# Kernel tuning notes

Measured on AMD Instinct MI355X. Metric: run time of the kernel, lower is better.

The kernel has to match this reference:

```python
import jax, jax.numpy as jnp
import numpy as np
from jax import lax

DG = 8  # deformable groups


def conv3(x, w, b):
    # 3x3 stride-1 SAME conv, NCHW/OIHW
    y = lax.conv_general_dilated(x, w, (1, 1), 'SAME',
                                 dimension_numbers=('NCHW', 'OIHW', 'NCHW'))
    return y + b[None, :, None, None]


def lrelu(x):
    return jnp.where(x >= 0, x, 0.1 * x)


def _mdcn(x, offset, mask, w, b, dg):
    """Modulated deformable conv v2: 3x3, stride 1, pad 1, dilation 1, groups 1.
    offset: [B, 2*dg*9, H, W] (first dg*9 = y offsets, second dg*9 = x offsets),
    mask:   [B, dg*9, H, W] (already sigmoided)."""
    B, C, H, W = x.shape
    kk = 9
    Cg = C // dg
    off = offset.reshape(B, 2, dg, kk, H, W)
    oy, ox = off[:, 0], off[:, 1]            # [B, dg, kk, H, W]
    m = mask.reshape(B, dg, kk, H, W)
    ky = (jnp.arange(kk) // 3 - 1).astype(x.dtype).reshape(1, 1, kk, 1, 1)
    kx = (jnp.arange(kk) % 3 - 1).astype(x.dtype).reshape(1, 1, kk, 1, 1)
    hg = jnp.arange(H, dtype=x.dtype).reshape(1, 1, 1, H, 1)
    wg = jnp.arange(W, dtype=x.dtype).reshape(1, 1, 1, 1, W)
    py = hg + ky + oy                        # sampling positions (pad=1 cancels k-1 shift)
    px = wg + kx + ox
    y0 = jnp.floor(py)
    x0 = jnp.floor(px)
    wy = py - y0
    wx = px - x0
    xg = x.reshape(B, dg, Cg, H * W)
    acc = jnp.zeros((B, dg, Cg, kk, H, W), x.dtype)
    for dy, dx, wgt in ((0.0, 0.0, (1 - wy) * (1 - wx)),
                        (0.0, 1.0, (1 - wy) * wx),
                        (1.0, 0.0, wy * (1 - wx)),
                        (1.0, 1.0, wy * wx)):
        yy = y0 + dy
        xx = x0 + dx
        valid = (yy >= 0) & (yy < H) & (xx >= 0) & (xx < W)
        yi = jnp.clip(yy, 0, H - 1).astype(jnp.int32)
        xi = jnp.clip(xx, 0, W - 1).astype(jnp.int32)
        idx = (yi * W + xi).reshape(B, dg, 1, kk * H * W)
        v = jnp.take_along_axis(xg, idx, axis=3).reshape(B, dg, Cg, kk, H, W)
        acc = acc + v * (wgt * valid.astype(x.dtype))[:, :, None]
    acc = acc * m[:, :, None]                # modulation mask
    sampled = acc.reshape(B, C, kk, H, W)
    out = jnp.einsum('bckhw,ock->bohw', sampled, w.reshape(w.shape[0], C, kk))
    return out + b[None, :, None, None]


def _dcn_pack(x, feat, w_om, b_om, w, b):
    out = conv3(feat, w_om, b_om)            # [B, 3*dg*9, H, W]
    o1, o2, mr = jnp.split(out, 3, axis=1)
    offset = jnp.concatenate([o1, o2], axis=1)
    mask = jax.nn.sigmoid(mr)
    return _mdcn(x, offset, mask, w, b, DG)


def _forward(ref, neb,
             w_oc1, b_oc1, w_om1, b_om1, w_dcn1, b_dcn1, w_fc, b_fc,
             w_cas1, b_cas1, w_cas2, b_cas2, w_om2, b_om2, w_dcn2, b_dcn2,
             w_ta1, b_ta1, w_ta2, b_ta2, w_ff, b_ff):
    start = ref
    # --- PCD alignment (nbr_feat_l = neb, ref_feat_l = ref) ---
    off = lrelu(conv3(jnp.concatenate([neb, ref], axis=1), w_oc1, b_oc1))
    feat = _dcn_pack(neb, off, w_om1, b_om1, w_dcn1, b_dcn1)
    feat = lrelu(conv3(feat, w_fc, b_fc))
    off = jnp.concatenate([feat, ref], axis=1)
    off = lrelu(conv3(lrelu(conv3(off, w_cas1, b_cas1)), w_cas2, b_cas2))
    feat = lrelu(_dcn_pack(feat, off, w_om2, b_om2, w_dcn2, b_dcn2))
    # --- TSA fusion (ref=ref, neb=feat) ---
    emb_ref = conv3(ref, w_ta1, b_ta1)
    emb = conv3(feat, w_ta2, b_ta2)
    corr = jnp.sum(emb * emb_ref, axis=1, keepdims=True)  # [B,1,H,W]
    feat = lrelu(conv3(ref * corr, w_ff, b_ff))
    return feat + start


def setup_inputs() -> dict:
    key = jax.random.key(0)
    ks = jax.random.split(key, 32)
    B, C, H, W = 4, 64, 180, 320
    s = 0.05
    p = lambda k, shape: (jax.random.normal(k, shape, jnp.float32) * s)
    OM = 3 * DG * 9  # 216
    return {
        'ref': jax.random.normal(ks[0], (B, C, H, W), jnp.float32),
        'neb': jax.random.normal(ks[1], (B, C, H, W), jnp.float32),
        'w_oc1': p(ks[2], (C, 2 * C, 3, 3)), 'b_oc1': p(ks[3], (C,)),
        'w_om1': p(ks[4], (OM, C, 3, 3)),    'b_om1': p(ks[5], (OM,)),
        'w_dcn1': p(ks[6], (C, C, 3, 3)),    'b_dcn1': p(ks[7], (C,)),
        'w_fc': p(ks[8], (C, C, 3, 3)),      'b_fc': p(ks[9], (C,)),
        'w_cas1': p(ks[10], (C, 2 * C, 3, 3)), 'b_cas1': p(ks[11], (C,)),
        'w_cas2': p(ks[12], (C, C, 3, 3)),   'b_cas2': p(ks[13], (C,)),
        'w_om2': p(ks[14], (OM, C, 3, 3)),   'b_om2': p(ks[15], (OM,)),
        'w_dcn2': p(ks[16], (C, C, 3, 3)),   'b_dcn2': p(ks[17], (C,)),
        'w_ta1': p(ks[18], (C, C, 3, 3)),    'b_ta1': p(ks[19], (C,)),
        'w_ta2': p(ks[20], (C, C, 3, 3)),    'b_ta2': p(ks[21], (C,)),
        'w_ff': p(ks[22], (C, C, 3, 3)),     'b_ff': p(ks[23], (C,)),
    }


def reference(ref, neb,
              w_oc1, b_oc1, w_om1, b_om1, w_dcn1, b_dcn1, w_fc, b_fc,
              w_cas1, b_cas1, w_cas2, b_cas2, w_om2, b_om2, w_dcn2, b_dcn2,
              w_ta1, b_ta1, w_ta2, b_ta2, w_ff, b_ff):
    return _forward(ref, neb,
                    w_oc1, b_oc1, w_om1, b_om1, w_dcn1, b_dcn1, w_fc, b_fc,
                    w_cas1, b_cas1, w_cas2, b_cas2, w_om2, b_om2, w_dcn2, b_dcn2,
                    w_ta1, b_ta1, w_ta2, b_ta2, w_ff, b_ff)
```

## Files before the change

### kernel.cpp

```cpp
#include <hip/hip_runtime.h>
#include <cmath>


using short8 = __attribute__((ext_vector_type(8))) short;
using f32x4  = __attribute__((ext_vector_type(4))) float;

#define DEVINL static __device__ __forceinline__

DEVINL unsigned short f2bf(float f){
    unsigned u = __float_as_uint(f);
    u += 0x7fffu + ((u >> 16) & 1u);
    return (unsigned short)(u >> 16);
}
DEVINL unsigned pack2(float a, float b){ return (unsigned)f2bf(a) | ((unsigned)f2bf(b) << 16); }
DEVINL float bflo(unsigned u){ return __uint_as_float(u << 16); }
DEVINL float bfhi(unsigned u){ return __uint_as_float(u & 0xffff0000u); }
DEVINL float bf2f(unsigned short u){ return __uint_as_float((unsigned)u << 16); }
DEVINL float lrelu_f(float v){ return v >= 0.f ? v : 0.1f * v; }

DEVINL void swz_decode(int& bx, int& by, int& bz){
    const int gx = gridDim.x, gy = gridDim.y;
    int lin = blockIdx.x + gx * (blockIdx.y + gy * blockIdx.z);
    int nwg = gx * gy * gridDim.z;
    int q = nwg >> 3, r = nwg & 7;
    int xcd = lin & 7, idx = lin >> 3;
    int swz = (xcd < r ? xcd * (q + 1) : r + xcd * q) + idx;
    bz = swz / (gx * gy);
    int rem = swz - bz * gx * gy;
    by = rem / gx; bx = rem - by * gx;
}

struct Ptr4 { unsigned short* p[4]; };

__global__ __launch_bounds__(256) void nchw2nhwc2(const float* __restrict__ inA,
                                                  const float* __restrict__ inB,
                                                  unsigned short* __restrict__ outA,
                                                  unsigned short* __restrict__ outB)
{
    constexpr int HW = 180 * 320;
    const int blk = blockIdx.x;
    const float* in = (blk < 900) ? inA : inB;
    unsigned short* out = (blk < 900) ? outA : outB;
    size_t idx = (size_t)(blk % 900) * 256 + threadIdx.x;
    size_t bb = idx / HW, p = idx % HW;
    const float* src = in + (bb * 64) * (size_t)HW + p;
    unsigned short* dst = out + idx * 64;
    #pragma unroll
    for (int c0 = 0; c0 < 64; c0 += 16) {
        unsigned r[8];
        #pragma unroll
        for (int q = 0; q < 8; ++q)
            r[q] = pack2(src[(size_t)(c0 + 2*q) * HW], src[(size_t)(c0 + 2*q + 1) * HW]);
        *(uint4*)(dst + c0)     = *(uint4*)&r[0];
        *(uint4*)(dst + c0 + 8) = *(uint4*)&r[4];
    }
}

struct PrepArgs {
    const float* src[11];
    unsigned short* dst[11];
    int cout[11]; int cin[11]; int nch[11]; int kind[11];
};

__global__ __launch_bounds__(256) void prep_all(PrepArgs a)
{
    const int t = blockIdx.y;
    const int idx = blockIdx.x * 256 + threadIdx.x;
    if (a.kind[t] == 1) {
        if (idx >= 36864) return;
        int kk = idx & 31, oc = (idx >> 5) & 63, s = idx >> 11;
        int k = s * 32 + kk;
        int gt = k >> 3, c8 = k & 7;
        int g = gt / 9, tp = gt - g * 9;
        a.dst[t][idx] = f2bf(a.src[t][((size_t)oc * 64 + g * 8 + c8) * 9 + tp]);
    } else {
        int cin = a.cin[t], cout = a.cout[t];
        int ncs = cin / 32;
        int total = a.nch[t] * 9 * ncs * 2048;
        if (idx >= total) return;
        int kk = idx & 31, oc_l = (idx >> 5) & 63, rest = idx >> 11;
        int cs = rest % ncs; int rest2 = rest / ncs;
        int j = rest2 % 9; int ch = rest2 / 9;
        int oc = ch * 64 + oc_l, c = cs * 32 + kk;
        float v = (oc < cout) ? a.src[t][((size_t)oc * cin + c) * 9 + j] : 0.f;
        a.dst[t][idx] = f2bf(v);
    }
}

template<int CIN, bool TWO_IN, bool ACT, bool SCALE, int OUTMODE, int NM>
__global__ __launch_bounds__(256, (CIN == 128 ? 2 : 3)) void conv_mfma(
    const unsigned short* __restrict__ in0, const unsigned short* __restrict__ in1,
    const unsigned short* __restrict__ wgt, const float* __restrict__ bias,
    unsigned short* __restrict__ out, const float* __restrict__ corr,
    const float* __restrict__ res, float* __restrict__ outf,
    Ptr4 omout, int choff, int zdiv, int COUT)
{
    constexpr int H = 180, W = 320, HW = H * W;
    constexpr int NCB = CIN / 8;
    constexpr int NCS = CIN / 32;
    __shared__ __align__(16) unsigned char lds[6 * 34 * CIN * 2];

    const int tid = threadIdx.x;
    int bx, by, bz;
    swz_decode(bx, by, bz);
    int b, ch;
    if (OUTMODE == 1) { b = bz / zdiv; ch = bz % zdiv + choff; }
    else              { b = bz; ch = 0; }
    const int x0 = bx * 32, y0 = by * 4;

    for (int t = tid; t < 6 * 34 * NCB; t += 256) {
        int cb = t % NCB; int r = t / NCB;
        int xp = r % 34, yp = r / 34;
        int gx = x0 - 1 + xp, gy = y0 - 1 + yp;
        uint4 v = make_uint4(0, 0, 0, 0);
        if (gx >= 0 && gx < W && gy >= 0 && gy < H) {
            size_t pix = (size_t)b * HW + (size_t)gy * W + gx;
            const unsigned short* src;
            if (TWO_IN) src = (cb < 8) ? (in0 + pix * 64 + cb * 8) : (in1 + pix * 64 + (cb - 8) * 8);
            else        src = in0 + pix * CIN + cb * 8;
            v = *(const uint4*)src;
            if (SCALE) {
                float cv = corr[pix];
                v.x = pack2(bflo(v.x) * cv, bfhi(v.x) * cv);
                v.y = pack2(bflo(v.y) * cv, bfhi(v.y) * cv);
                v.z = pack2(bflo(v.z) * cv, bfhi(v.z) * cv);
                v.w = pack2(bflo(v.w) * cv, bfhi(v.w) * cv);
            }
        }
        int blk = cb ^ (xp & 7);
        *(uint4*)&lds[(size_t)((yp * 34 + xp) * NCB + blk) * 16] = v;
    }
    __syncthreads();

    const int wv = tid >> 6, lane = tid & 63;
    const int ll = lane & 15, lh = lane >> 4;
    const unsigned short* wchunk = wgt + (size_t)ch * (9 * NCS * 2048);
    const int alane = ll * 32 + lh * 8;

    f32x4 acc[NM][2];
    #pragma unroll
    for (int mi = 0; mi < NM; ++mi)
        #pragma unroll
        for (int nf = 0; nf < 2; ++nf) acc[mi][nf] = f32x4{0.f, 0.f, 0.f, 0.f};

    #pragma unroll
    for (int j = 0; j < 9; ++j) {
        const int jy = j / 3, jx = j % 3;
        #pragma unroll
        for (int cs = 0; cs < NCS; ++cs) {
            const int s = j * NCS + cs;
            short8 a[NM];
            #pragma unroll
            for (int mi = 0; mi < NM; ++mi)
                a[mi] = *(const short8*)(wchunk + (size_t)s * 2048 + mi * 512 + alane);
            short8 bf[2];
            #pragma unroll
            for (int nf = 0; nf < 2; ++nf) {
                int xp = nf * 16 + ll + jx;
                int blk = (cs * 4 + lh) ^ (xp & 7);
                int addr = (((wv + jy) * 34 + xp) * NCB + blk) * 16;
                bf[nf] = *(const short8*)&lds[addr];
            }
            #pragma unroll
            for (int mi = 0; mi < NM; ++mi)
                #pragma unroll
                for (int nf = 0; nf < 2; ++nf)
                    acc[mi][nf] = __builtin_amdgcn_mfma_f32_16x16x32_bf16(a[mi], bf[nf], acc[mi][nf], 0, 0, 0);
        }
    }

    const int py = y0 + wv;
    const size_t pixrow = (size_t)b * HW + (size_t)py * W;
    #pragma unroll
    for (int nf = 0; nf < 2; ++nf) {
        const int px = x0 + nf * 16 + ll;
        if (OUTMODE == 3) {
            float dot = 0.f;
            const unsigned* er = (const unsigned*)(in1 + (pixrow + px) * 64);
            #pragma unroll
            for (int mi = 0; mi < NM; ++mi) {
                const int oc_l = mi * 16 + lh * 4;
                unsigned e0 = er[oc_l / 2], e1 = er[oc_l / 2 + 1];
                float t0 = acc[mi][nf][0] + bias[oc_l + 0];
                float t1 = acc[mi][nf][1] + bias[oc_l + 1];
                float t2 = acc[mi][nf][2] + bias[oc_l + 2];
                float t3 = acc[mi][nf][3] + bias[oc_l + 3];
                dot += t0 * bflo(e0) + t1 * bfhi(e0) + t2 * bflo(e1) + t3 * bfhi(e1);
            }
            dot += __shfl_xor(dot, 16);
            dot += __shfl_xor(dot, 32);
            if (lh == 0) outf[pixrow + px] = dot;
        } else if (OUTMODE == 1) {
            unsigned short* oslot = omout.p[b];
            #pragma unroll
            for (int mi = 0; mi < NM; ++mi) {
                const int oc_l = mi * 16 + lh * 4;
                #pragma unroll
                for (int jj = 0; jj < 4; ++jj) {
                    int ocg = ch * 64 + oc_l + jj;
                    if (ocg < COUT) {
                        float t = acc[mi][nf][jj] + bias[ocg];
                        oslot[(size_t)ocg * HW + (size_t)py * W + px] = f2bf(ACT ? lrelu_f(t) : t);
                    }
                }
            }
        } else {
            #pragma unroll
            for (int mi = 0; mi < NM; ++mi) {
                const int oc_l = mi * 16 + lh * 4;
                if (OUTMODE == 0) {
                    float v[4];
                    #pragma unroll
                    for (int jj = 0; jj < 4; ++jj) {
                        float t = acc[mi][nf][jj] + bias[oc_l + jj];
                        v[jj] = ACT ? lrelu_f(t) : t;
                    }
                    uint2 st; st.x = pack2(v[0], v[1]); st.y = pack2(v[2], v[3]);
                    *(uint2*)&out[(pixrow + px) * 64 + oc_l] = st;
                } else {
                    #pragma unroll
                    for (int jj = 0; jj < 4; ++jj) {
                        int oc = oc_l + jj;
                        float t = acc[mi][nf][jj] + bias[oc];
                        if (ACT) t = lrelu_f(t);
                        size_t idx = ((size_t)b * 64 + oc) * HW + (size_t)py * W + px;
                        outf[idx] = t + res[idx];
                    }
                }
            }
        }
    }
}

template<int ACT>
__global__ __launch_bounds__(256, 4) void mdcn_mfma(
    const unsigned short* __restrict__ x, size_t xstride,
    const unsigned short* __restrict__ om, size_t omstride,
    const unsigned short* __restrict__ wgt, const float* __restrict__ bias,
    unsigned short* __restrict__ out, size_t ostride)
{
    constexpr int H = 180, W = 320, HW = H * W;
    __shared__ __align__(16) unsigned char sv[72 * 32 * 16];

    const int tid = threadIdx.x;
    int bx, by, bz;
    swz_decode(bx, by, bz);
    const unsigned short* xb  = x  + (size_t)bz * xstride;
    const unsigned short* omb = om + (size_t)bz * omstride;
    unsigned short* ob        = out + (size_t)bz * ostride;
    const int px0 = bx * 32;
    const int py  = by;

    {
        const int pxl = tid & 31, g = tid >> 5;
        const int px = px0 + pxl;
        const size_t p = (size_t)py * W + px;
        const unsigned short* omg = omb + (size_t)(g * 9) * HW + p;

        float oyv[9], oxv[9], mmv[9];
        #pragma unroll
        for (int k = 0; k < 9; ++k) oyv[k] = bf2f(omg[(size_t)k * HW]);
        #pragma unroll
        for (int k = 0; k < 9; ++k) oxv[k] = bf2f(omg[(size_t)(72 + k) * HW]);
        #pragma unroll
        for (int k = 0; k < 9; ++k) mmv[k] = bf2f(omg[(size_t)(144 + k) * HW]);

        #pragma unroll
        for (int k = 0; k < 9; ++k) {
            float m = 1.f / (1.f + __expf(-mmv[k]));
            float pyf = (float)(py + (k / 3) - 1) + oyv[k];
            float pxf = (float)(px + (k % 3) - 1) + oxv[k];
            float y0f = floorf(pyf), x0f = floorf(pxf);
            float wy = pyf - y0f, wx = pxf - x0f;
            int yi = (int)y0f, xi = (int)x0f;
            bool vy0 = (yi >= 0) && (yi < H);
            bool vy1 = (yi + 1 >= 0) && (yi + 1 < H);
            bool vx0 = (xi >= 0) && (xi < W);
            bool vx1 = (xi + 1 >= 0) && (xi + 1 < W);
            float w00 = (vy0 && vx0) ? (1.f - wy) * (1.f - wx) * m : 0.f;
            float w01 = (vy0 && vx1) ? (1.f - wy) * wx * m : 0.f;
            float w10 = (vy1 && vx0) ? wy * (1.f - wx) * m : 0.f;
            float w11 = (vy1 && vx1) ? wy * wx * m : 0.f;
            int yc0 = min(max(yi, 0), H - 1), yc1 = min(max(yi + 1, 0), H - 1);
            int xc0 = min(max(xi, 0), W - 1), xc1 = min(max(xi + 1, 0), W - 1);
            uint4 c00 = *(const uint4*)(xb + ((size_t)(yc0 * W + xc0) * 64 + g * 8));
            uint4 c01 = *(const uint4*)(xb + ((size_t)(yc0 * W + xc1) * 64 + g * 8));
            uint4 c10 = *(const uint4*)(xb + ((size_t)(yc1 * W + xc0) * 64 + g * 8));
            uint4 c11 = *(const uint4*)(xb + ((size_t)(yc1 * W + xc1) * 64 + g * 8));
            const unsigned* p00 = (const unsigned*)&c00;
            const unsigned* p01 = (const unsigned*)&c01;
            const unsigned* p10 = (const unsigned*)&c10;
            const unsigned* p11 = (const unsigned*)&c11;
            unsigned r[4];
            #pragma unroll
            for (int q = 0; q < 4; ++q) {
                float lo = w00 * bflo(p00[q]) + w01 * bflo(p01[q]) + w10 * bflo(p10[q]) + w11 * bflo(p11[q]);
                float hi = w00 * bfhi(p00[q]) + w01 * bfhi(p01[q]) + w10 * bfhi(p10[q]) + w11 * bfhi(p11[q]);
                r[q] = pack2(lo, hi);
            }
            *(uint4*)&sv[(size_t)((g * 9 + k) * 32 + pxl) * 16] = *(uint4*)r;
        }
    }
    __syncthreads();

    const int wv = tid >> 6, lane = tid & 63;
    const int ll = lane & 15, lh = lane >> 4;
    f32x4 acc[2] = {f32x4{0.f,0.f,0.f,0.f}, f32x4{0.f,0.f,0.f,0.f}};
    #pragma unroll
    for (int s = 0; s < 18; ++s) {
        short8 a = *(const short8*)(wgt + (size_t)(s * 64 + wv * 16 + ll) * 32 + lh * 8);
        #pragma unroll
        for (int nf = 0; nf < 2; ++nf) {
            short8 bb = *(const short8*)&sv[(size_t)s * 2048 + lh * 512 + (nf * 16 + ll) * 16];
            acc[nf] = __builtin_amdgcn_mfma_f32_16x16x32_bf16(a, bb, acc[nf], 0, 0, 0);
        }
    }
    #pragma unroll
    for (int nf = 0; nf < 2; ++nf) {
        int opx = px0 + nf * 16 + ll;
        int oc0 = wv * 16 + lh * 4;
        float v[4];
        #pragma unroll
        for (int jj = 0; jj < 4; ++jj) {
            float t = acc[nf][jj] + bias[oc0 + jj];
            v[jj] = ACT ? lrelu_f(t) : t;
        }
        uint2 st; st.x = pack2(v[0], v[1]); st.y = pack2(v[2], v[3]);
        *(uint2*)&ob[((size_t)py * W + opx) * 64 + oc0] = st;
    }
}

extern "C" void kernel_launch(void* const* d_in, const int* in_sizes, int n_in,
                              void* d_out, int out_size, void* d_ws, size_t ws_size,
                              hipStream_t stream)
{
    const float* ref    = (const float*)d_in[0];
    const float* neb    = (const float*)d_in[1];
    const float* w_oc1  = (const float*)d_in[2];  const float* b_oc1  = (const float*)d_in[3];
    const float* w_om1  = (const float*)d_in[4];  const float* b_om1  = (const float*)d_in[5];
    const float* w_dcn1 = (const float*)d_in[6];  const float* b_dcn1 = (const float*)d_in[7];
    const float* w_fc   = (const float*)d_in[8];  const float* b_fc   = (const float*)d_in[9];
    const float* w_cas1 = (const float*)d_in[10]; const float* b_cas1 = (const float*)d_in[11];
    const float* w_cas2 = (const float*)d_in[12]; const float* b_cas2 = (const float*)d_in[13];
    const float* w_om2  = (const float*)d_in[14]; const float* b_om2  = (const float*)d_in[15];
    const float* w_dcn2 = (const float*)d_in[16]; const float* b_dcn2 = (const float*)d_in[17];
    const float* w_ta1  = (const float*)d_in[18]; const float* b_ta1  = (const float*)d_in[19];
    const float* w_ta2  = (const float*)d_in[20]; const float* b_ta2  = (const float*)d_in[21];
    const float* w_ff   = (const float*)d_in[22]; const float* b_ff   = (const float*)d_in[23];

    constexpr int H = 180, W = 320, HW = H * W;
    constexpr size_t CHW = (size_t)HW * 64;
    constexpr size_t SLB = 4 * CHW * 2;
    constexpr size_t OMSLOT_EL = (size_t)HW * 216;
    constexpr size_t OMSLOT_B  = OMSLOT_EL * 2;

    char* wsb = (char*)d_ws;
    unsigned short* S0 = (unsigned short*)(wsb);
    unsigned short* S1 = (unsigned short*)(wsb + SLB);
    unsigned short* S2 = (unsigned short*)(wsb + 2 * SLB);
    unsigned short* S3 = (unsigned short*)(wsb + 3 * SLB);
    float* corrf = (float*)S3;
    unsigned short* ffw = (unsigned short*)(wsb + SLB + (2u << 20));

    char* doutb = (char*)d_out;
    unsigned short* omA0 = (unsigned short*)doutb;
    unsigned short* omA1 = omA0 + OMSLOT_EL;
    unsigned short* wb   = (unsigned short*)(doutb + 2 * OMSLOT_B);
    const bool big = ws_size >= 4 * SLB + 2 * OMSLOT_B;
    unsigned short* omB0 = (unsigned short*)(wsb + 4 * SLB);
    unsigned short* omB1 = omB0 + OMSLOT_EL;

    unsigned short* w_oc1p = wb + 0;
    unsigned short* w_om1p = wb + 73728;
    unsigned short* w_dcn1p= wb + 221184;
    unsigned short* w_fcp  = wb + 258048;
    unsigned short* w_cas1p= wb + 294912;
    unsigned short* w_cas2p= wb + 368640;
    unsigned short* w_om2p = wb + 405504;
    unsigned short* w_dcn2p= wb + 552960;
    unsigned short* w_ta1p = wb + 589824;
    unsigned short* w_ta2p = wb + 626688;
    unsigned short* w_ffp  = wb + 663552;

    dim3 blk(256);
    dim3 g4(10, 45, 4);
    dim3 gm(10, 180, 2);
    Ptr4 none{};

    nchw2nhwc2<<<1800, blk, 0, stream>>>(ref, neb, S0, S1);

    {
        PrepArgs pa;
        const float* srcs[11] = {w_oc1, w_om1, w_dcn1, w_fc, w_cas1, w_cas2, w_om2, w_dcn2, w_ta1, w_ta2, w_ff};
        unsigned short* dsts[11] = {w_oc1p, w_om1p, w_dcn1p, w_fcp, w_cas1p, w_cas2p, w_om2p, w_dcn2p, w_ta1p, w_ta2p, w_ffp};
        int couts[11] = {64, 216, 0, 64, 64, 64, 216, 0, 64, 64, 64};
        int cins[11]  = {128, 64, 0, 64, 128, 64, 64, 0, 64, 64, 64};
        int nchs[11]  = {1, 4, 0, 1, 1, 1, 4, 0, 1, 1, 1};
        int kinds[11] = {0, 0, 1, 0, 0, 0, 0, 1, 0, 0, 0};
        for (int i = 0; i < 11; ++i) {
            pa.src[i] = srcs[i]; pa.dst[i] = dsts[i];
            pa.cout[i] = couts[i]; pa.cin[i] = cins[i]; pa.nch[i] = nchs[i]; pa.kind[i] = kinds[i];
        }
        prep_all<<<dim3(576, 11), blk, 0, stream>>>(pa);
    }

    conv_mfma<128, true, true, false, 0, 4><<<g4, blk, 0, stream>>>(
        S1, S0, w_oc1p, b_oc1, S2, nullptr, nullptr, nullptr, none, 0, 1, 64);

    auto ompack = [&](const unsigned short* inp, const unsigned short* wp, const float* bp,
                      Ptr4 slots, int nb){
        conv_mfma<64, false, false, false, 1, 4><<<dim3(10, 45, 3 * nb), blk, 0, stream>>>(
            inp, nullptr, wp, bp, nullptr, nullptr, nullptr, nullptr, slots, 0, 3, 216);
        conv_mfma<64, false, false, false, 1, 2><<<dim3(10, 45, nb), blk, 0, stream>>>(
            inp, nullptr, wp, bp, nullptr, nullptr, nullptr, nullptr, slots, 3, 1, 216);
    };

    if (big) {
        Ptr4 slots{omA0, omA1, omB0, omB1};
        ompack(S2, w_om1p, b_om1, slots, 4);
        mdcn_mfma<0><<<gm, blk, 0, stream>>>(S1, CHW, omA0, OMSLOT_EL, w_dcn1p, b_dcn1, S3, CHW);
        mdcn_mfma<0><<<gm, blk, 0, stream>>>(S1 + 2 * CHW, CHW, omB0, OMSLOT_EL, w_dcn1p, b_dcn1, S3 + 2 * CHW, CHW);
    } else {
        Ptr4 slots{omA0, omA1, nullptr, nullptr};
        for (int pp = 0; pp < 2; ++pp) {
            ompack(S2 + 2 * pp * CHW, w_om1p, b_om1, slots, 2);
            mdcn_mfma<0><<<gm, blk, 0, stream>>>(S1 + 2 * pp * CHW, CHW, omA0, OMSLOT_EL,
                                                 w_dcn1p, b_dcn1, S3 + 2 * pp * CHW, CHW);
        }
    }

    conv_mfma<64, false, true, false, 0, 4><<<g4, blk, 0, stream>>>(
        S3, nullptr, w_fcp, b_fc, S2, nullptr, nullptr, nullptr, none, 0, 1, 64);
    conv_mfma<128, true, true, false, 0, 4><<<g4, blk, 0, stream>>>(
        S2, S0, w_cas1p, b_cas1, S1, nullptr, nullptr, nullptr, none, 0, 1, 64);
    conv_mfma<64, false, true, false, 0, 4><<<g4, blk, 0, stream>>>(
        S1, nullptr, w_cas2p, b_cas2, S3, nullptr, nullptr, nullptr, none, 0, 1, 64);

    if (big) {
        Ptr4 slots{omA0, omA1, omB0, omB1};
        ompack(S3, w_om2p, b_om2, slots, 4);
        mdcn_mfma<1><<<gm, blk, 0, stream>>>(S2, CHW, omA0, OMSLOT_EL, w_dcn2p, b_dcn2, S1, CHW);
        mdcn_mfma<1><<<gm, blk, 0, stream>>>(S2 + 2 * CHW, CHW, omB0, OMSLOT_EL, w_dcn2p, b_dcn2, S1 + 2 * CHW, CHW);
    } else {
        Ptr4 slots{omA0, omA1, nullptr, nullptr};
        for (int pp = 0; pp < 2; ++pp) {
            ompack(S3 + 2 * pp * CHW, w_om2p, b_om2, slots, 2);
            mdcn_mfma<1><<<gm, blk, 0, stream>>>(S2 + 2 * pp * CHW, CHW, omA0, OMSLOT_EL,
                                                 w_dcn2p, b_dcn2, S1 + 2 * pp * CHW, CHW);
        }
    }

    conv_mfma<64, false, false, false, 0, 4><<<g4, blk, 0, stream>>>(
        S0, nullptr, w_ta1p, b_ta1, S2, nullptr, nullptr, nullptr, none, 0, 1, 64);
    conv_mfma<64, false, false, false, 3, 4><<<g4, blk, 0, stream>>>(
        S1, S2, w_ta2p, b_ta2, nullptr, nullptr, nullptr, corrf, none, 0, 1, 64);

    hipMemcpyAsync(ffw, w_ffp, 36864 * 2, hipMemcpyDeviceToDevice, stream);

    conv_mfma<64, false, true, true, 2, 4><<<g4, blk, 0, stream>>>(
        S0, nullptr, ffw, b_ff, nullptr, corrf, ref, (float*)d_out, none, 0, 1, 64);
}
```

Measured before the change: 1.185 ms.

## Widen conv tiles, fuse temporal-attention convs, merge mdcn launches

Adds an NF template parameter so the 64-channel convs cover 64-pixel-wide tiles (4 N-fragments) with half as many blocks in x. This reuses each weight load across more MFMAs and cuts halo overhead. The two temporal-attention convs and their dot product are fused into one kernel, so the intermediate embedding no longer makes a round trip through memory. The paired mdcn launches become a single launch that takes per-batch offset-slot pointers. The trade-off is more accumulator registers and LDS per block, which may lower occupancy.

Result: faster. 1.157 ms (-2.4%).

```diff
diff --git a/kernel.cpp b/kernel.cpp
--- a/kernel.cpp
+++ b/kernel.cpp
@@ -87,7 +87,7 @@
     }
 }
 
-template<int CIN, bool TWO_IN, bool ACT, bool SCALE, int OUTMODE, int NM>
+template<int CIN, bool TWO_IN, bool ACT, bool SCALE, int OUTMODE, int NM, int NF>
 __global__ __launch_bounds__(256, (CIN == 128 ? 2 : 3)) void conv_mfma(
     const unsigned short* __restrict__ in0, const unsigned short* __restrict__ in1,
     const unsigned short* __restrict__ wgt, const float* __restrict__ bias,
@@ -98,7 +98,8 @@
     constexpr int H = 180, W = 320, HW = H * W;
     constexpr int NCB = CIN / 8;
     constexpr int NCS = CIN / 32;
-    __shared__ __align__(16) unsigned char lds[6 * 34 * CIN * 2];
+    constexpr int XW  = NF * 16 + 2;
+    __shared__ __align__(16) unsigned char lds[6 * XW * CIN * 2];
 
     const int tid = threadIdx.x;
     int bx, by, bz;
@@ -106,11 +107,11 @@
     int b, ch;
     if (OUTMODE == 1) { b = bz / zdiv; ch = bz % zdiv + choff; }
     else              { b = bz; ch = 0; }
-    const int x0 = bx * 32, y0 = by * 4;
-
-    for (int t = tid; t < 6 * 34 * NCB; t += 256) {
+    const int x0 = bx * (NF * 16), y0 = by * 4;
+
+    for (int t = tid; t < 6 * XW * NCB; t += 256) {
         int cb = t % NCB; int r = t / NCB;
-        int xp = r % 34, yp = r / 34;
+        int xp = r % XW, yp = r / XW;
         int gx = x0 - 1 + xp, gy = y0 - 1 + yp;
         uint4 v = make_uint4(0, 0, 0, 0);
         if (gx >= 0 && gx < W && gy >= 0 && gy < H) {
@@ -128,7 +129,7 @@
             }
         }
         int blk = cb ^ (xp & 7);
-        *(uint4*)&lds[(size_t)((yp * 34 + xp) * NCB + blk) * 16] = v;
+        *(uint4*)&lds[(size_t)((yp * XW + xp) * NCB + blk) * 16] = v;
     }
     __syncthreads();
 
@@ -137,11 +138,11 @@
     const unsigned short* wchunk = wgt + (size_t)ch * (9 * NCS * 2048);
     const int alane = ll * 32 + lh * 8;
 
-    f32x4 acc[NM][2];
+    f32x4 acc[NM][NF];
     #pragma unroll
     for (int mi = 0; mi < NM; ++mi)
         #pragma unroll
-        for (int nf = 0; nf < 2; ++nf) acc[mi][nf] = f32x4{0.f, 0.f, 0.f, 0.f};
+        for (int nf = 0; nf < NF; ++nf) acc[mi][nf] = f32x4{0.f, 0.f, 0.f, 0.f};
 
     #pragma unroll
     for (int j = 0; j < 9; ++j) {
@@ -153,18 +154,18 @@
             #pragma unroll
             for (int mi = 0; mi < NM; ++mi)
                 a[mi] = *(const short8*)(wchunk + (size_t)s * 2048 + mi * 512 + alane);
-            short8 bf[2];
-            #pragma unroll
-            for (int nf = 0; nf < 2; ++nf) {
+            short8 bf[NF];
+            #pragma unroll
+            for (int nf = 0; nf < NF; ++nf) {
                 int xp = nf * 16 + ll + jx;
                 int blk = (cs * 4 + lh) ^ (xp & 7);
-                int addr = (((wv + jy) * 34 + xp) * NCB + blk) * 16;
+                int addr = (((wv + jy) * XW + xp) * NCB + blk) * 16;
                 bf[nf] = *(const short8*)&lds[addr];
             }
             #pragma unroll
             for (int mi = 0; mi < NM; ++mi)
                 #pragma unroll
-                for (int nf = 0; nf < 2; ++nf)
+                for (int nf = 0; nf < NF; ++nf)
                     acc[mi][nf] = __builtin_amdgcn_mfma_f32_16x16x32_bf16(a[mi], bf[nf], acc[mi][nf], 0, 0, 0);
         }
     }
@@ -172,25 +173,9 @@
     const int py = y0 + wv;
     const size_t pixrow = (size_t)b * HW + (size_t)py * W;
     #pragma unroll
-    for (int nf = 0; nf < 2; ++nf) {
+    for (int nf = 0; nf < NF; ++nf) {
         const int px = x0 + nf * 16 + ll;
-        if (OUTMODE == 3) {
-            float dot = 0.f;
-            const unsigned* er = (const unsigned*)(in1 + (pixrow + px) * 64);
-            #pragma unroll
-            for (int mi = 0; mi < NM; ++mi) {
-                const int oc_l = mi * 16 + lh * 4;
-                unsigned e0 = er[oc_l / 2], e1 = er[oc_l / 2 + 1];
-                float t0 = acc[mi][nf][0] + bias[oc_l + 0];
-                float t1 = acc[mi][nf][1] + bias[oc_l + 1];
-                float t2 = acc[mi][nf][2] + bias[oc_l + 2];
-                float t3 = acc[mi][nf][3] + bias[oc_l + 3];
-                dot += t0 * bflo(e0) + t1 * bfhi(e0) + t2 * bflo(e1) + t3 * bfhi(e1);
-            }
-            dot += __shfl_xor(dot, 16);
-            dot += __shfl_xor(dot, 32);
-            if (lh == 0) outf[pixrow + px] = dot;
-        } else if (OUTMODE == 1) {
+        if (OUTMODE == 1) {
             unsigned short* oslot = omout.p[b];
             #pragma unroll
             for (int mi = 0; mi < NM; ++mi) {
@@ -232,22 +217,112 @@
     }
 }
 
-template<int ACT>
-__global__ __launch_bounds__(256, 4) void mdcn_mfma(
-    const unsigned short* __restrict__ x, size_t xstride,
-    const unsigned short* __restrict__ om, size_t omstride,
-    const unsigned short* __restrict__ wgt, const float* __restrict__ bias,
-    unsigned short* __restrict__ out, size_t ostride)
+__global__ __launch_bounds__(256, 3) void tacorr_mfma(
+    const unsigned short* __restrict__ inR,
+    const unsigned short* __restrict__ inE,
+    const unsigned short* __restrict__ wR, const float* __restrict__ bR,
+    const unsigned short* __restrict__ wE, const float* __restrict__ bE,
+    float* __restrict__ outf)
 {
     constexpr int H = 180, W = 320, HW = H * W;
-    __shared__ __align__(16) unsigned char sv[72 * 32 * 16];
+    constexpr int NE1 = 6 * 34 * 8;
+    __shared__ __align__(16) unsigned char lds[2][6 * 34 * 64 * 2];
 
     const int tid = threadIdx.x;
     int bx, by, bz;
     swz_decode(bx, by, bz);
-    const unsigned short* xb  = x  + (size_t)bz * xstride;
-    const unsigned short* omb = om + (size_t)bz * omstride;
-    unsigned short* ob        = out + (size_t)bz * ostride;
+    const int b = bz;
+    const int x0 = bx * 32, y0 = by * 4;
+
+    for (int t = tid; t < 2 * NE1; t += 256) {
+        int half = t / NE1, e = t - half * NE1;
+        int cb = e & 7; int r = e >> 3;
+        int xp = r % 34, yp = r / 34;
+        int gx = x0 - 1 + xp, gy = y0 - 1 + yp;
+        uint4 v = make_uint4(0, 0, 0, 0);
+        if (gx >= 0 && gx < W && gy >= 0 && gy < H) {
+            size_t pix = (size_t)b * HW + (size_t)gy * W + gx;
+            const unsigned short* src = (half ? inE : inR) + pix * 64 + cb * 8;
+            v = *(const uint4*)src;
+        }
+        int blk = cb ^ (xp & 7);
+        *(uint4*)&lds[half][(size_t)((yp * 34 + xp) * 8 + blk) * 16] = v;
+    }
+    __syncthreads();
+
+    const int wv = tid >> 6, lane = tid & 63;
+    const int ll = lane & 15, lh = lane >> 4;
+    const int alane = ll * 32 + lh * 8;
+
+    f32x4 accR[4][2], accE[4][2];
+    #pragma unroll
+    for (int mi = 0; mi < 4; ++mi)
+        #pragma unroll
+        for (int nf = 0; nf < 2; ++nf) { accR[mi][nf] = f32x4{0,0,0,0}; accE[mi][nf] = f32x4{0,0,0,0}; }
+
+    #pragma unroll
+    for (int j = 0; j < 9; ++j) {
+        const int jy = j / 3, jx = j % 3;
+        #pragma unroll
+        for (int cs = 0; cs < 2; ++cs) {
+            const int s = j * 2 + cs;
+            short8 aR[4], aE[4];
+            #pragma unroll
+            for (int mi = 0; mi < 4; ++mi) {
+                aR[mi] = *(const short8*)(wR + (size_t)s * 2048 + mi * 512 + alane);
+                aE[mi] = *(const short8*)(wE + (size_t)s * 2048 + mi * 512 + alane);
+            }
+            #pragma unroll
+            for (int nf = 0; nf < 2; ++nf) {
+                int xp = nf * 16 + ll + jx;
+                int blk = (cs * 4 + lh) ^ (xp & 7);
+                int addr = (((wv + jy) * 34 + xp) * 8 + blk) * 16;
+                short8 bfR = *(const short8*)&lds[0][addr];
+                short8 bfE = *(const short8*)&lds[1][addr];
+                #pragma unroll
+                for (int mi = 0; mi < 4; ++mi) {
+                    accR[mi][nf] = __builtin_amdgcn_mfma_f32_16x16x32_bf16(aR[mi], bfR, accR[mi][nf], 0, 0, 0);
+                    accE[mi][nf] = __builtin_amdgcn_mfma_f32_16x16x32_bf16(aE[mi], bfE, accE[mi][nf], 0, 0, 0);
+                }
+            }
+        }
+    }
+
+    const int py = y0 + wv;
+    const size_t pixrow = (size_t)b * HW + (size_t)py * W;
+    #pragma unroll
+    for (int nf = 0; nf < 2; ++nf) {
+        const int px = x0 + nf * 16 + ll;
+        float dot = 0.f;
+        #pragma unroll
+        for (int mi = 0; mi < 4; ++mi) {
+            const int oc_l = mi * 16 + lh * 4;
+            #pragma unroll
+            for (int jj = 0; jj < 4; ++jj)
+                dot += (accR[mi][nf][jj] + bR[oc_l + jj]) * (accE[mi][nf][jj] + bE[oc_l + jj]);
+        }
+        dot += __shfl_xor(dot, 16);
+        dot += __shfl_xor(dot, 32);
+        if (lh == 0) outf[pixrow + px] = dot;
+    }
+}
+
+template<int ACT>
+__global__ __launch_bounds__(256, 4) void mdcn_mfma(
+    const unsigned short* __restrict__ x, Ptr4 omslots,
+    const unsigned short* __restrict__ wgt, const float* __restrict__ bias,
+    unsigned short* __restrict__ out)
+{
+    constexpr int H = 180, W = 320, HW = H * W;
+    constexpr size_t CHW = (size_t)HW * 64;
+    __shared__ __align__(16) unsigned char sv[72 * 32 * 16];
+
+    const int tid = threadIdx.x;
+    int bx, by, bz;
+    swz_decode(bx, by, bz);
+    const unsigned short* xb  = x + (size_t)bz * CHW;
+    const unsigned short* omb = omslots.p[bz];
+    unsigned short* ob        = out + (size_t)bz * CHW;
     const int px0 = bx * 32;
     const int py  = by;
 
@@ -384,7 +459,7 @@
 
     dim3 blk(256);
     dim3 g4(10, 45, 4);
-    dim3 gm(10, 180, 2);
+    dim3 g4w(5, 45, 4);
     Ptr4 none{};
 
     nchw2nhwc2<<<1800, blk, 0, stream>>>(ref, neb, S0, S1);
@@ -404,59 +479,54 @@
         prep_all<<<dim3(576, 11), blk, 0, stream>>>(pa);
     }
 
-    conv_mfma<128, true, true, false, 0, 4><<<g4, blk, 0, stream>>>(
+    conv_mfma<128, true, true, false, 0, 4, 2><<<g4, blk, 0, stream>>>(
         S1, S0, w_oc1p, b_oc1, S2, nullptr, nullptr, nullptr, none, 0, 1, 64);
 
     auto ompack = [&](const unsigned short* inp, const unsigned short* wp, const float* bp,
                       Ptr4 slots, int nb){
-        conv_mfma<64, false, false, false, 1, 4><<<dim3(10, 45, 3 * nb), blk, 0, stream>>>(
+        conv_mfma<64, false, false, false, 1, 4, 4><<<dim3(5, 45, 3 * nb), blk, 0, stream>>>(
             inp, nullptr, wp, bp, nullptr, nullptr, nullptr, nullptr, slots, 0, 3, 216);
-        conv_mfma<64, false, false, false, 1, 2><<<dim3(10, 45, nb), blk, 0, stream>>>(
+        conv_mfma<64, false, false, false, 1, 2, 4><<<dim3(5, 45, nb), blk, 0, stream>>>(
             inp, nullptr, wp, bp, nullptr, nullptr, nullptr, nullptr, slots, 3, 1, 216);
     };
 
     if (big) {
         Ptr4 slots{omA0, omA1, omB0, omB1};
         ompack(S2, w_om1p, b_om1, slots, 4);
-        mdcn_mfma<0><<<gm, blk, 0, stream>>>(S1, CHW, omA0, OMSLOT_EL, w_dcn1p, b_dcn1, S3, CHW);
-        mdcn_mfma<0><<<gm, blk, 0, stream>>>(S1 + 2 * CHW, CHW, omB0, OMSLOT_EL, w_dcn1p, b_dcn1, S3 + 2 * CHW, CHW);
+        mdcn_mfma<0><<<dim3(10, 180, 4), blk, 0, stream>>>(S1, slots, w_dcn1p, b_dcn1, S3);
     } else {
         Ptr4 slots{omA0, omA1, nullptr, nullptr};
         for (int pp = 0; pp < 2; ++pp) {
             ompack(S2 + 2 * pp * CHW, w_om1p, b_om1, slots, 2);
-            mdcn_mfma<0><<<gm, blk, 0, stream>>>(S1 + 2 * pp * CHW, CHW, omA0, OMSLOT_EL,
-                                                 w_dcn1p, b_dcn1, S3 + 2 * pp * CHW, CHW);
-        }
-    }
-
-    conv_mfma<64, false, true, false, 0, 4><<<g4, blk, 0, stream>>>(
+            mdcn_mfma<0><<<dim3(10, 180, 2), blk, 0, stream>>>(S1 + 2 * pp * CHW, slots,
+                                                               w_dcn1p, b_dcn1, S3 + 2 * pp * CHW);
+        }
+    }
+
+    conv_mfma<64, false, true, false, 0, 4, 4><<<g4w, blk, 0, stream>>>(
         S3, nullptr, w_fcp, b_fc, S2, nullptr, nullptr, nullptr, none, 0, 1, 64);
-    conv_mfma<128, true, true, false, 0, 4><<<g4, blk, 0, stream>>>(
+    conv_mfma<128, true, true, false, 0, 4, 2><<<g4, blk, 0, stream>>>(
         S2, S0, w_cas1p, b_cas1, S1, nullptr, nullptr, nullptr, none, 0, 1, 64);
-    conv_mfma<64, false, true, false, 0, 4><<<g4, blk, 0, stream>>>(
+    conv_mfma<64, false, true, false, 0, 4, 4><<<g4w, blk, 0, stream>>>(
         S1, nullptr, w_cas2p, b_cas2, S3, nullptr, nullptr, nullptr, none, 0, 1, 64);
 
     if (big) {
         Ptr4 slots{omA0, omA1, omB0, omB1};
         ompack(S3, w_om2p, b_om2, slots, 4);
-        mdcn_mfma<1><<<gm, blk, 0, stream>>>(S2, CHW, omA0, OMSLOT_EL, w_dcn2p, b_dcn2, S1, CHW);
-        mdcn_mfma<1><<<gm, blk, 0, stream>>>(S2 + 2 * CHW, CHW, omB0, OMSLOT_EL, w_dcn2p, b_dcn2, S1 + 2 * CHW, CHW);
+        mdcn_mfma<1><<<dim3(10, 180, 4), blk, 0, stream>>>(S2, slots, w_dcn2p, b_dcn2, S1);
     } else {
         Ptr4 slots{omA0, omA1, nullptr, nullptr};
         for (int pp = 0; pp < 2; ++pp) {
             ompack(S3 + 2 * pp * CHW, w_om2p, b_om2, slots, 2);
-            mdcn_mfma<1><<<gm, blk, 0, stream>>>(S2 + 2 * pp * CHW, CHW, omA0, OMSLOT_EL,
-                                                 w_dcn2p, b_dcn2, S1 + 2 * pp * CHW, CHW);
-        }
-    }
-
-    conv_mfma<64, false, false, false, 0, 4><<<g4, blk, 0, stream>>>(
-        S0, nullptr, w_ta1p, b_ta1, S2, nullptr, nullptr, nullptr, none, 0, 1, 64);
-    conv_mfma<64, false, false, false, 3, 4><<<g4, blk, 0, stream>>>(
-        S1, S2, w_ta2p, b_ta2, nullptr, nullptr, nullptr, corrf, none, 0, 1, 64);
+            mdcn_mfma<1><<<dim3(10, 180, 2), blk, 0, stream>>>(S2 + 2 * pp * CHW, slots,
+                                                               w_dcn2p, b_dcn2, S1 + 2 * pp * CHW);
+        }
+    }
+
+    tacorr_mfma<<<g4, blk, 0, stream>>>(S0, S1, w_ta1p, b_ta1, w_ta2p, b_ta2, corrf);
 
     hipMemcpyAsync(ffw, w_ffp, 36864 * 2, hipMemcpyDeviceToDevice, stream);
 
-    conv_mfma<64, false, true, true, 2, 4><<<g4, blk, 0, stream>>>(
+    conv_mfma<64, false, true, true, 2, 4, 4><<<g4w, blk, 0, stream>>>(
         S0, nullptr, ffw, b_ff, nullptr, corrf, ref, (float*)d_out, none, 0, 1, 64);
 }
```
